# Kernel tuning notes

Measured on AMD Instinct MI355X. Metric: run time of the kernel, lower is better.

## Reference

```python
import jax, jax.numpy as jnp
import numpy as np

B, D_IN, D_H = 8192, 1024, 1024


def setup_inputs() -> dict:
    key = jax.random.key(0)
    k = jax.random.split(key, 7)
    s_h = 1.0 / np.sqrt(D_H)
    s_x = 1.0 / np.sqrt(D_IN)
    return {
        "x": jax.random.normal(k[0], (B, D_IN), jnp.float32),
        "h": jax.random.normal(k[1], (B, D_H), jnp.float32),
        "c": jax.random.normal(k[2], (B, D_H), jnp.float32),
        "Wh_w": jax.random.uniform(k[3], (D_H, D_H), jnp.float32, -s_h, s_h),
        "Wh_b": jax.random.uniform(k[4], (D_H,), jnp.float32, -s_h, s_h),
        "Wx_w": jax.random.uniform(k[5], (D_H, D_IN), jnp.float32, -s_x, s_x),
        "Wx_b": jax.random.uniform(k[6], (D_H,), jnp.float32, -s_x, s_x),
    }


def reference(x, h, c, Wh_w, Wh_b, Wx_w, Wx_b):
    # Source reuses the same Wh/Wx for all four gates, so the pre-activation
    # z is identical across gates: i = f = o = sigmoid(z), g = tanh(z).
    z = h @ Wh_w.T + Wh_b + x @ Wx_w.T + Wx_b  # [B, D_H]
    s = jax.nn.sigmoid(z)                      # i = f = o
    g = jnp.tanh(z)
    c_new = s * c + s * g
    h_new = s * jnp.tanh(c_new)
    return (h_new, c_new)
```

## Files before the change

### kernel.cpp

```cpp
#include <hip/hip_runtime.h>
#include <stdint.h>
#include <stddef.h>


typedef __attribute__((ext_vector_type(8))) short bf16x8;
typedef __attribute__((ext_vector_type(4))) float f32x4;
typedef __attribute__((ext_vector_type(8))) unsigned short ushort8;

#define BATCH 8192
#define DH    1024
#define KTOT  2048

__device__ __forceinline__ unsigned short f2bf(float f) {
    unsigned int u = __float_as_uint(f);
    u += 0x7FFFu + ((u >> 16) & 1u);
    return (unsigned short)(u >> 16);
}

__device__ __forceinline__ float tanh_fast(float v) {
    float a = fabsf(v);
    float e = __expf(-2.0f * a);
    float t = (1.0f - e) / (1.0f + e);
    return v < 0.0f ? -t : t;
}

__device__ __forceinline__ void gload_lds16(const void* g, void* l) {
    __builtin_amdgcn_global_load_lds(
        (const __attribute__((address_space(1))) void*)g,
        (__attribute__((address_space(3))) void*)l, 16, 0, 0);
}

__global__ __launch_bounds__(256) void cast_cat_kernel(
    const float* __restrict__ s0, const float* __restrict__ s1,
    unsigned short* __restrict__ dst)
{
    unsigned int idx  = blockIdx.x * 256u + threadIdx.x;
    unsigned int base = idx * 8u;
    unsigned int r    = base >> 11;
    unsigned int k    = base & 2047u;
    const float* src = (k < 1024u) ? (s0 + (size_t)r * 1024u + k)
                                   : (s1 + (size_t)r * 1024u + (k - 1024u));
    const float4* s4 = (const float4*)src;
    float4 f0 = s4[0], f1 = s4[1];
    ushort8 o;
    o[0] = f2bf(f0.x); o[1] = f2bf(f0.y); o[2] = f2bf(f0.z); o[3] = f2bf(f0.w);
    o[4] = f2bf(f1.x); o[5] = f2bf(f1.y); o[6] = f2bf(f1.z); o[7] = f2bf(f1.w);
    *(ushort8*)(dst + base) = o;
}

#define BK 64
__global__ __launch_bounds__(256) void lstm_gemm_kernel(
    const unsigned short* __restrict__ A,
    const unsigned short* __restrict__ W,
    const float* __restrict__ Whb, const float* __restrict__ Wxb,
    const float* __restrict__ Cin,
    float* __restrict__ Hout, float* __restrict__ Cout)
{
    __shared__ unsigned short tA[128 * BK];
    __shared__ unsigned short tB[128 * BK];

    const int tid  = threadIdx.x;
    const int wid  = tid >> 6;
    const int lane = tid & 63;
    const int bidN = blockIdx.x & 7;
    const int bidM = blockIdx.x >> 3;
    const int row0 = bidM * 128;
    const int col0 = bidN * 128;
    const int wm = (wid >> 1) * 64;
    const int wn = (wid & 1) * 64;

    f32x4 acc[4][4] = {};

    const int lrow = lane >> 3;
    const int lcol = (lane & 7) * 8;

    for (int kt = 0; kt < KTOT / BK; ++kt) {
        const int k0 = kt * BK;
        #pragma unroll
        for (int i = 0; i < 4; ++i) {
            const int ch = wid * 4 + i;
            const int rr = ch * 8 + lrow;
            gload_lds16(A + (size_t)(row0 + rr) * KTOT + k0 + lcol, &tA[ch * 512]);
            gload_lds16(W + (size_t)(col0 + rr) * KTOT + k0 + lcol, &tB[ch * 512]);
        }
        __syncthreads();

        #pragma unroll
        for (int kk = 0; kk < 2; ++kk) {
            bf16x8 af[4], bfr[4];
            #pragma unroll
            for (int m = 0; m < 4; ++m)
                af[m] = *(const bf16x8*)&tA[(wm + m * 16 + (lane & 15)) * BK + kk * 32 + (lane >> 4) * 8];
            #pragma unroll
            for (int n = 0; n < 4; ++n)
                bfr[n] = *(const bf16x8*)&tB[(wn + n * 16 + (lane & 15)) * BK + kk * 32 + (lane >> 4) * 8];
            #pragma unroll
            for (int m = 0; m < 4; ++m)
                #pragma unroll
                for (int n = 0; n < 4; ++n)
                    acc[m][n] = __builtin_amdgcn_mfma_f32_16x16x32_bf16(af[m], bfr[n], acc[m][n], 0, 0, 0);
        }
        __syncthreads();
    }

    const int rlo = (lane >> 4) * 4;
    const int cc  = lane & 15;
    #pragma unroll
    for (int n = 0; n < 4; ++n) {
        const int col  = col0 + wn + n * 16 + cc;
        const float bias = Whb[col] + Wxb[col];
        #pragma unroll
        for (int m = 0; m < 4; ++m) {
            #pragma unroll
            for (int j = 0; j < 4; ++j) {
                const int row = row0 + wm + m * 16 + rlo + j;
                const size_t off = (size_t)row * DH + col;
                const float z = acc[m][n][j] + bias;
                const float s = 0.5f + 0.5f * tanh_fast(0.5f * z);
                const float g = tanh_fast(z);
                const float cn = s * (Cin[off] + g);
                const float hn = s * tanh_fast(cn);
                Hout[off] = hn;
                Cout[off] = cn;
            }
        }
    }
}

__global__ __launch_bounds__(256) void lstm_naive_kernel(
    const float* __restrict__ x, const float* __restrict__ h,
    const float* __restrict__ c,
    const float* __restrict__ Whw, const float* __restrict__ Whb,
    const float* __restrict__ Wxw, const float* __restrict__ Wxb,
    float* __restrict__ Hout, float* __restrict__ Cout)
{
    const int idx = blockIdx.x * 256 + threadIdx.x;
    const int b = idx >> 10, n = idx & 1023;
    const float* hr = h  + (size_t)b * 1024;
    const float* xr = x  + (size_t)b * 1024;
    const float* wh = Whw + (size_t)n * 1024;
    const float* wx = Wxw + (size_t)n * 1024;
    float z = Whb[n] + Wxb[n];
    for (int k = 0; k < 1024; ++k) z += hr[k] * wh[k] + xr[k] * wx[k];
    const float s = 0.5f + 0.5f * tanh_fast(0.5f * z);
    const float g = tanh_fast(z);
    const size_t off = (size_t)b * 1024 + n;
    const float cn = s * (c[off] + g);
    Hout[off] = s * tanh_fast(cn);
    Cout[off] = cn;
}

extern "C" void kernel_launch(void* const* d_in, const int* in_sizes, int n_in,
                              void* d_out, int out_size, void* d_ws, size_t ws_size,
                              hipStream_t stream) {
    const float* x   = (const float*)d_in[0];
    const float* h   = (const float*)d_in[1];
    const float* c   = (const float*)d_in[2];
    const float* Whw = (const float*)d_in[3];
    const float* Whb = (const float*)d_in[4];
    const float* Wxw = (const float*)d_in[5];
    const float* Wxb = (const float*)d_in[6];
    float* Hout = (float*)d_out;
    float* Cout = Hout + (size_t)BATCH * DH;

    const size_t needA = (size_t)BATCH * KTOT * 2;
    const size_t needW = (size_t)DH * KTOT * 2;

    if (ws_size >= needA + needW) {
        unsigned short* Abf = (unsigned short*)d_ws;
        unsigned short* Wbf = (unsigned short*)((char*)d_ws + needA);
        cast_cat_kernel<<<8192, 256, 0, stream>>>(h, x, Abf);
        cast_cat_kernel<<<1024, 256, 0, stream>>>(Whw, Wxw, Wbf);
        lstm_gemm_kernel<<<512, 256, 0, stream>>>(Abf, Wbf, Whb, Wxb, c, Hout, Cout);
    } else {
        lstm_naive_kernel<<<(BATCH * DH) / 256, 256, 0, stream>>>(
            x, h, c, Whw, Whb, Wxw, Wxb, Hout, Cout);
    }
}
```

Measured before the change: 272.1 us.

## Triple-buffer LDS GEMM with 256x128 tiles, swizzle, and fused cast kernel

Replaces the single-buffered 128x128 GEMM with a 256x128 tile over 512 threads. It uses a three-slot LDS ring: global-to-LDS loads for k-tile kt+2 are issued in phases interleaved with the MFMA work on tile kt, using vmcnt waits, barriers and setprio. An XOR swizzle on LDS columns aims to reduce bank conflicts. The two cast launches are merged into one grid-stride kernel. In exchange, LDS use is much larger (about 144KB) and only 256 blocks are launched, which limits occupancy and wave-level parallelism.

```diff
diff --git a/kernel.cpp b/kernel.cpp
--- a/kernel.cpp
+++ b/kernel.cpp
@@ -10,6 +10,10 @@
 #define BATCH 8192
 #define DH    1024
 #define KTOT  2048
+#define NKT   32
+#define ASLOT 16384
+#define BSLOT 8192
+#define LDS_BYTES ((3*ASLOT + 3*BSLOT) * 2)
 
 __device__ __forceinline__ unsigned short f2bf(float f) {
     unsigned int u = __float_as_uint(f);
@@ -30,97 +34,159 @@
         (__attribute__((address_space(3))) void*)l, 16, 0, 0);
 }
 
-__global__ __launch_bounds__(256) void cast_cat_kernel(
-    const float* __restrict__ s0, const float* __restrict__ s1,
-    unsigned short* __restrict__ dst)
-{
-    unsigned int idx  = blockIdx.x * 256u + threadIdx.x;
-    unsigned int base = idx * 8u;
-    unsigned int r    = base >> 11;
-    unsigned int k    = base & 2047u;
-    const float* src = (k < 1024u) ? (s0 + (size_t)r * 1024u + k)
-                                   : (s1 + (size_t)r * 1024u + (k - 1024u));
-    const float4* s4 = (const float4*)src;
-    float4 f0 = s4[0], f1 = s4[1];
-    ushort8 o;
-    o[0] = f2bf(f0.x); o[1] = f2bf(f0.y); o[2] = f2bf(f0.z); o[3] = f2bf(f0.w);
-    o[4] = f2bf(f1.x); o[5] = f2bf(f1.y); o[6] = f2bf(f1.z); o[7] = f2bf(f1.w);
-    *(ushort8*)(dst + base) = o;
-}
-
-#define BK 64
-__global__ __launch_bounds__(256) void lstm_gemm_kernel(
+#define A_CHUNKS 2097152u
+#define W_CHUNKS 262144u
+__global__ __launch_bounds__(256) void cast_all_kernel(
+    const float* __restrict__ h, const float* __restrict__ x,
+    const float* __restrict__ Whw, const float* __restrict__ Wxw,
+    unsigned short* __restrict__ Abf, unsigned short* __restrict__ Wbf)
+{
+    for (unsigned c = blockIdx.x * 256u + threadIdx.x;
+         c < A_CHUNKS + W_CHUNKS; c += gridDim.x * 256u) {
+        const float* src;
+        unsigned short* dst;
+        if (c < A_CHUNKS) {
+            unsigned base = c * 8u, r = base >> 11, k = base & 2047u;
+            src = (k < 1024u) ? (h + (size_t)r * 1024u + k)
+                              : (x + (size_t)r * 1024u + (k - 1024u));
+            dst = Abf + base;
+        } else {
+            unsigned c2 = c - A_CHUNKS;
+            unsigned base = c2 * 8u, r = base >> 11, k = base & 2047u;
+            src = (k < 1024u) ? (Whw + (size_t)r * 1024u + k)
+                              : (Wxw + (size_t)r * 1024u + (k - 1024u));
+            dst = Wbf + base;
+        }
+        const float4* s4 = (const float4*)src;
+        float4 f0 = s4[0], f1 = s4[1];
+        ushort8 o;
+        o[0]=f2bf(f0.x); o[1]=f2bf(f0.y); o[2]=f2bf(f0.z); o[3]=f2bf(f0.w);
+        o[4]=f2bf(f1.x); o[5]=f2bf(f1.y); o[6]=f2bf(f1.z); o[7]=f2bf(f1.w);
+        *(ushort8*)dst = o;
+    }
+}
+
+template <int KK, int MG, bool READB, typename F>
+__device__ __forceinline__ void phase_fn(
+    const unsigned short* As, const unsigned short* Bs,
+    int wr, int wc, int ln15, int hi, int ln7,
+    f32x4 (&acc)[8][2], bf16x8 (&bfr)[2], F&& mid)
+{
+    bf16x8 af[4];
+    #pragma unroll
+    for (int i = 0; i < 4; ++i) {
+        int r = wr * 128 + (MG * 4 + i) * 16 + ln15;
+        af[i] = *(const bf16x8*)(As + r * 64 + (((KK * 4 + hi) ^ ln7) * 8));
+    }
+    if constexpr (READB) {
+        #pragma unroll
+        for (int n = 0; n < 2; ++n) {
+            int r = wc * 32 + n * 16 + ln15;
+            bfr[n] = *(const bf16x8*)(Bs + r * 64 + (((KK * 4 + hi) ^ ln7) * 8));
+        }
+    }
+    mid();
+    __builtin_amdgcn_s_barrier();
+    asm volatile("s_waitcnt lgkmcnt(0)" ::: "memory");
+    __builtin_amdgcn_sched_barrier(0);
+    __builtin_amdgcn_s_setprio(1);
+    #pragma unroll
+    for (int i = 0; i < 4; ++i)
+        #pragma unroll
+        for (int n = 0; n < 2; ++n)
+            acc[MG * 4 + i][n] = __builtin_amdgcn_mfma_f32_16x16x32_bf16(
+                af[i], bfr[n], acc[MG * 4 + i][n], 0, 0, 0);
+    __builtin_amdgcn_s_setprio(0);
+    __builtin_amdgcn_s_barrier();
+}
+
+__global__ __launch_bounds__(512, 2) void lstm_gemm_kernel(
     const unsigned short* __restrict__ A,
     const unsigned short* __restrict__ W,
     const float* __restrict__ Whb, const float* __restrict__ Wxb,
     const float* __restrict__ Cin,
     float* __restrict__ Hout, float* __restrict__ Cout)
 {
-    __shared__ unsigned short tA[128 * BK];
-    __shared__ unsigned short tB[128 * BK];
+    extern __shared__ unsigned short smem[];
+    unsigned short* sA = smem;
+    unsigned short* sB = smem + 3 * ASLOT;
 
     const int tid  = threadIdx.x;
     const int wid  = tid >> 6;
     const int lane = tid & 63;
+    const int wr = wid >> 2, wc = wid & 3;
     const int bidN = blockIdx.x & 7;
     const int bidM = blockIdx.x >> 3;
-    const int row0 = bidM * 128;
-    const int col0 = bidN * 128;
-    const int wm = (wid >> 1) * 64;
-    const int wn = (wid & 1) * 64;
-
-    f32x4 acc[4][4] = {};
-
-    const int lrow = lane >> 3;
-    const int lcol = (lane & 7) * 8;
-
-    for (int kt = 0; kt < KTOT / BK; ++kt) {
-        const int k0 = kt * BK;
-        #pragma unroll
-        for (int i = 0; i < 4; ++i) {
-            const int ch = wid * 4 + i;
-            const int rr = ch * 8 + lrow;
-            gload_lds16(A + (size_t)(row0 + rr) * KTOT + k0 + lcol, &tA[ch * 512]);
-            gload_lds16(W + (size_t)(col0 + rr) * KTOT + k0 + lcol, &tB[ch * 512]);
-        }
-        __syncthreads();
-
-        #pragma unroll
-        for (int kk = 0; kk < 2; ++kk) {
-            bf16x8 af[4], bfr[4];
-            #pragma unroll
-            for (int m = 0; m < 4; ++m)
-                af[m] = *(const bf16x8*)&tA[(wm + m * 16 + (lane & 15)) * BK + kk * 32 + (lane >> 4) * 8];
-            #pragma unroll
-            for (int n = 0; n < 4; ++n)
-                bfr[n] = *(const bf16x8*)&tB[(wn + n * 16 + (lane & 15)) * BK + kk * 32 + (lane >> 4) * 8];
-            #pragma unroll
-            for (int m = 0; m < 4; ++m)
-                #pragma unroll
-                for (int n = 0; n < 4; ++n)
-                    acc[m][n] = __builtin_amdgcn_mfma_f32_16x16x32_bf16(af[m], bfr[n], acc[m][n], 0, 0, 0);
-        }
-        __syncthreads();
-    }
-
-    const int rlo = (lane >> 4) * 4;
-    const int cc  = lane & 15;
+    const int row0 = bidM * 256, col0 = bidN * 128;
+    const int ln15 = lane & 15, hi = lane >> 4, ln7 = lane & 7;
+
+    const unsigned short* Ag = A + (size_t)row0 * KTOT;
+    const unsigned short* Bg = W + (size_t)col0 * KTOT;
+
+    f32x4 acc[8][2] = {};
+    bf16x8 bfr[2];
+
+    auto stage = [&](const unsigned short* gbase, unsigned short* lbase) {
+        #pragma unroll
+        for (int j = 0; j < 2; ++j) {
+            int c = j * 512 + tid;
+            int r = c >> 3, p = c & 7;
+            const unsigned short* g = gbase + (size_t)r * KTOT + ((p ^ (r & 7)) * 8);
+            unsigned short* l = lbase + (size_t)(j * 512 + wid * 64) * 8;
+            gload_lds16(g, l);
+        }
+    };
+
+    stage(Ag,                         sA);
+    stage(Ag + (size_t)128 * KTOT,    sA + 8192);
+    stage(Bg,                         sB);
+    stage(Ag + 64,                    sA + ASLOT);
+    stage(Ag + (size_t)128 * KTOT + 64, sA + ASLOT + 8192);
+    stage(Bg + 64,                    sB + BSLOT);
+    asm volatile("s_waitcnt vmcnt(6)" ::: "memory");
+    __builtin_amdgcn_s_barrier();
+
+    int scur = 0, swr = 2;
+    for (int kt = 0; kt < NKT; ++kt) {
+        const unsigned short* As = sA + scur * ASLOT;
+        const unsigned short* Bs = sB + scur * BSLOT;
+        unsigned short* Aw = sA + swr * ASLOT;
+        unsigned short* Bw = sB + swr * BSLOT;
+        const size_t kn = (size_t)(kt + 2) * 64;
+        const bool pre = (kt < NKT - 2);
+
+        phase_fn<0, 0, true >(As, Bs, wr, wc, ln15, hi, ln7, acc, bfr,
+            [&] { if (pre) stage(Ag + kn, Aw); });
+        phase_fn<0, 1, false>(As, Bs, wr, wc, ln15, hi, ln7, acc, bfr,
+            [&] { if (pre) stage(Ag + (size_t)128 * KTOT + kn, Aw + 8192); });
+        phase_fn<1, 0, true >(As, Bs, wr, wc, ln15, hi, ln7, acc, bfr,
+            [&] { if (pre) stage(Bg + kn, Bw); });
+        phase_fn<1, 1, false>(As, Bs, wr, wc, ln15, hi, ln7, acc, bfr,
+            [&] {
+                if (kt < NKT - 2)       asm volatile("s_waitcnt vmcnt(6)" ::: "memory");
+                else if (kt == NKT - 2) asm volatile("s_waitcnt vmcnt(0)" ::: "memory");
+            });
+
+        scur = (scur == 2) ? 0 : scur + 1;
+        swr  = (swr  == 2) ? 0 : swr  + 1;
+    }
+
+    const int rlo = hi * 4;
     #pragma unroll
-    for (int n = 0; n < 4; ++n) {
-        const int col  = col0 + wn + n * 16 + cc;
+    for (int n = 0; n < 2; ++n) {
+        const int col = col0 + wc * 32 + n * 16 + ln15;
         const float bias = Whb[col] + Wxb[col];
         #pragma unroll
-        for (int m = 0; m < 4; ++m) {
+        for (int m = 0; m < 8; ++m) {
             #pragma unroll
             for (int j = 0; j < 4; ++j) {
-                const int row = row0 + wm + m * 16 + rlo + j;
+                const int row = row0 + wr * 128 + m * 16 + rlo + j;
                 const size_t off = (size_t)row * DH + col;
                 const float z = acc[m][n][j] + bias;
                 const float s = 0.5f + 0.5f * tanh_fast(0.5f * z);
                 const float g = tanh_fast(z);
                 const float cn = s * (Cin[off] + g);
-                const float hn = s * tanh_fast(cn);
-                Hout[off] = hn;
+                Hout[off] = s * tanh_fast(cn);
                 Cout[off] = cn;
             }
         }
@@ -169,9 +235,12 @@
     if (ws_size >= needA + needW) {
         unsigned short* Abf = (unsigned short*)d_ws;
         unsigned short* Wbf = (unsigned short*)((char*)d_ws + needA);
-        cast_cat_kernel<<<8192, 256, 0, stream>>>(h, x, Abf);
-        cast_cat_kernel<<<1024, 256, 0, stream>>>(Whw, Wxw, Wbf);
-        lstm_gemm_kernel<<<512, 256, 0, stream>>>(Abf, Wbf, Whb, Wxb, c, Hout, Cout);
+        cast_all_kernel<<<2304, 256, 0, stream>>>(h, x, Whw, Wxw, Abf, Wbf);
+        (void)hipFuncSetAttribute((const void*)lstm_gemm_kernel,
+                                  hipFuncAttributeMaxDynamicSharedMemorySize,
+                                  LDS_BYTES);
+        lstm_gemm_kernel<<<256, 512, LDS_BYTES, stream>>>(
+            Abf, Wbf, Whb, Wxb, c, Hout, Cout);
     } else {
         lstm_naive_kernel<<<(BATCH * DH) / 256, 256, 0, stream>>>(
             x, h, c, Whw, Whb, Wxw, Wxb, Hout, Cout);
```

New measurement: 224.4 us. 1.21x faster.
